# Kernel optimization log

Measured on AMD Instinct MI355X. Metric: run time of the kernel, lower is better.

Reference implementation:

```python
import jax, jax.numpy as jnp
from jax import lax
import numpy as np

OBJECT_W, BCE_W, DICE_W = 2.0, 5.0, 5.0
B, N, M, C = 8, 128, 32, 65536


def setup_inputs() -> dict:
    key = jax.random.key(0)
    k1, k2, k3 = jax.random.split(key, 3)
    objectness = jax.random.normal(k1, (B, N), jnp.float32)
    pred_masks = jax.random.normal(k2, (B, N, C), jnp.float32)
    gt_masks = jax.random.randint(k3, (B, M, C), 0, 2).astype(jnp.float32)
    return {"objectness": objectness, "pred_masks": pred_masks, "gt_masks": gt_masks}


def _cost_matrices(objectness, pred, gt):
    # BCE-with-logits vs all-ones target: log(1+exp(-x)) = softplus(-x)
    # BCE-with-logits vs all-zeros target: softplus(x)
    sp_pos = jax.nn.softplus(-pred)                       # [B,N,C]
    sp_neg = jax.nn.softplus(pred)                        # [B,N,C]
    # einsum('nc,mc->nm', pos, t) + einsum('nc,mc->nm', neg, 1-t), batched.
    # neg @ (1-t) = neg.sum(c) - neg @ t (avoids materializing 1-t).
    bce = (jnp.einsum('bnc,bmc->bnm', sp_pos, gt)
           + sp_neg.sum(-1)[:, :, None]
           - jnp.einsum('bnc,bmc->bnm', sp_neg, gt)) / pred.shape[-1]
    s = jax.nn.sigmoid(pred)
    numerator = 2.0 * jnp.einsum('bnc,bmc->bnm', s, gt)
    denominator = s.sum(-1)[:, :, None] + gt.sum(-1)[:, None, :]
    dice = 1.0 - (numerator + 1.0) / (denominator + 1.0)
    obj = -jax.nn.sigmoid(objectness)[:, :, None]         # [B,N,1]
    return OBJECT_W * obj + BCE_W * bce + DICE_W * dice    # [B,N,M]


def _lsap(cost):
    """Jonker-Volgenant shortest-augmenting-path LSAP (scipy algorithm).
    cost: [R, C] with R <= C. Returns col4row [R] int32: column per row."""
    R, Cn = cost.shape
    BIG = jnp.float32(1e30)

    def outer(cur_row, carry):
        u, v, row4col, col4row = carry
        shortest = jnp.full((Cn,), BIG, jnp.float32)
        path = jnp.full((Cn,), -1, jnp.int32)
        SR = jnp.zeros((R,), bool)
        SC = jnp.zeros((Cn,), bool)

        def sp_cond(s):
            return s[6] < 0

        def sp_body(s):
            i, shortest, path, SR, SC, minVal, sink = s
            SR = SR.at[i].set(True)
            d = minVal + cost[i] - u[i] - v
            better = (d < shortest) & (~SC)
            shortest = jnp.where(better, d, shortest)
            path = jnp.where(better, i, path)
            masked = jnp.where(SC, BIG, shortest)
            j = jnp.argmin(masked).astype(jnp.int32)
            minVal = masked[j]
            SC = SC.at[j].set(True)
            nxt = row4col[j]
            sink = jnp.where(nxt == -1, j, jnp.int32(-1))
            i = jnp.where(nxt == -1, i, nxt)
            return (i, shortest, path, SR, SC, minVal, sink)

        init = (cur_row.astype(jnp.int32), shortest, path, SR, SC,
                jnp.float32(0.0), jnp.int32(-1))
        i, shortest, path, SR, SC, minVal, sink = lax.while_loop(sp_cond, sp_body, init)

        # dual updates (scipy rectangular_lsap)
        u = u.at[cur_row].add(minVal)
        extra = SR & (jnp.arange(R) != cur_row)
        sp_at_col = shortest[jnp.clip(col4row, 0, Cn - 1)]
        u = jnp.where(extra, u + minVal - sp_at_col, u)
        v = jnp.where(SC, v - (minVal - shortest), v)

        # augment along path
        def aug_cond(s):
            return ~s[3]

        def aug_body(s):
            j, row4col, col4row, done = s
            i = path[j]
            row4col = row4col.at[j].set(i)
            tmp = col4row[i]
            col4row = col4row.at[i].set(j)
            done = (i == cur_row)
            return (tmp, row4col, col4row, done)

        _, row4col, col4row, _ = lax.while_loop(
            aug_cond, aug_body, (sink, row4col, col4row, jnp.array(False)))
        return (u, v, row4col, col4row)

    carry = (jnp.zeros((R,), jnp.float32), jnp.zeros((Cn,), jnp.float32),
             jnp.full((Cn,), -1, jnp.int32), jnp.full((R,), -1, jnp.int32))
    u, v, row4col, col4row = lax.fori_loop(0, R, outer, carry)
    return col4row


def reference(objectness, pred_masks, gt_masks):
    cost = _cost_matrices(objectness, pred_masks, gt_masks)   # [B,N,M]
    # scipy lsap on [N,M] then sort by target == solving on cost.T [M,N]:
    # indices[b, m] = matched query index for target m.
    indices = jax.vmap(_lsap)(jnp.transpose(cost, (0, 2, 1)))  # [B,M]
    return cost, indices
```

## Files before the change

kernel.cpp:

```cpp
#include <hip/hip_runtime.h>
#include <hip/hip_bf16.h>

#define LOG2E 1.4426950408889634f
#define LN2   0.6931471805599453f

typedef __attribute__((ext_vector_type(8))) short short8;
typedef __attribute__((ext_vector_type(4))) float f32x4;

#define B_ 8
#define N_ 128
#define M_ 32
#define C_ 65536
#define KCHUNKS 32
#define KC (C_ / KCHUNKS)
#define BK 128
#define AST 136

__device__ __forceinline__ unsigned short f2bf(float f) {
  unsigned u = __builtin_bit_cast(unsigned, f);
  u += 0x7fffu + ((u >> 16) & 1u);
  return (unsigned short)(u >> 16);
}
__device__ __forceinline__ unsigned pack_rne(float lo, float hi) {
  return (unsigned)f2bf(lo) | ((unsigned)f2bf(hi) << 16);
}
__device__ __forceinline__ unsigned pack_trunc(float lo, float hi) {
  unsigned ul = __builtin_bit_cast(unsigned, lo);
  unsigned uh = __builtin_bit_cast(unsigned, hi);
  return (uh & 0xFFFF0000u) | (ul >> 16);
}

__global__ __launch_bounds__(512, 2) void cost_partial_kernel(
    const float* __restrict__ pred, const float* __restrict__ gt,
    float* __restrict__ xg, float* __restrict__ sg,
    float* __restrict__ spsum, float* __restrict__ ssum,
    float* __restrict__ gtsum)
{
  __shared__ unsigned short Asx[128 * AST];
  __shared__ unsigned short Ass[128 * AST];
  __shared__ unsigned short Bt[32 * AST];
  const int kc = blockIdx.x, b = blockIdx.y;
  const int tid = threadIdx.x;
  const int lane = tid & 63;
  const int wave = tid >> 6;
  const int quad = lane >> 4, lcol = lane & 15;
  const int prow = tid >> 2, pq = tid & 3;
  const int grow = tid >> 4, gh = tid & 15;
  const int c0 = kc * KC;

  const float* predB = pred + (size_t)b * N_ * C_ + (size_t)prow * C_ + c0;
  const float* gtB   = gt   + (size_t)b * M_ * C_ + (size_t)grow * C_ + c0;

  float spacc = 0.f, sacc = 0.f, gtacc = 0.f;
  f32x4 acc[2][2];
#pragma unroll
  for (int rt = 0; rt < 2; ++rt)
#pragma unroll
    for (int ct = 0; ct < 2; ++ct)
      acc[rt][ct] = (f32x4){0.f, 0.f, 0.f, 0.f};

  for (int ks = 0; ks < KC / BK; ++ks) {
    const int cb = ks * BK;
    float4 p[8];
#pragma unroll
    for (int i = 0; i < 8; ++i)
      p[i] = *(const float4*)(predB + cb + (i * 4 + pq) * 4);
    float4 g0 = *(const float4*)(gtB + cb + gh * 4);
    float4 g1 = *(const float4*)(gtB + cb + (gh + 16) * 4);

#pragma unroll
    for (int i = 0; i < 8; ++i) {
      float xs[4] = {p[i].x, p[i].y, p[i].z, p[i].w};
      float ss[4];
#pragma unroll
      for (int e = 0; e < 4; ++e) {
        float x = xs[e];
        float t = fminf(fmaxf(x * LOG2E, -80.f), 80.f);
        float e2 = __builtin_amdgcn_exp2f(t);
        float z = 1.f + e2;
        float s = e2 * __builtin_amdgcn_rcpf(z);
        spacc += __builtin_amdgcn_logf(z) * LN2;
        sacc += s;
        ss[e] = s;
      }
      uint2 ux = {pack_rne(xs[0], xs[1]), pack_rne(xs[2], xs[3])};
      uint2 us = {pack_rne(ss[0], ss[1]), pack_rne(ss[2], ss[3])};
      *(uint2*)&Asx[prow * AST + (i * 4 + pq) * 4] = ux;
      *(uint2*)&Ass[prow * AST + (i * 4 + pq) * 4] = us;
    }
    gtacc += g0.x + g0.y + g0.z + g0.w + g1.x + g1.y + g1.z + g1.w;
    *(uint2*)&Bt[grow * AST + gh * 4]      = (uint2){pack_trunc(g0.x, g0.y), pack_trunc(g0.z, g0.w)};
    *(uint2*)&Bt[grow * AST + 64 + gh * 4] = (uint2){pack_trunc(g1.x, g1.y), pack_trunc(g1.z, g1.w)};
    __syncthreads();

    const unsigned short* Abase = (wave < 4) ? &Asx[(wave * 32) * AST]
                                             : &Ass[((wave - 4) * 32) * AST];
#pragma unroll
    for (int k0 = 0; k0 < BK; k0 += 32) {
      const int koff = k0 + quad * 8;
      short8 bf0 = *(const short8*)&Bt[lcol * AST + koff];
      short8 bf1 = *(const short8*)&Bt[(16 + lcol) * AST + koff];
#pragma unroll
      for (int rt = 0; rt < 2; ++rt) {
        short8 af = *(const short8*)&Abase[(rt * 16 + lcol) * AST + koff];
        acc[rt][0] = __builtin_amdgcn_mfma_f32_16x16x32_bf16(af, bf0, acc[rt][0], 0, 0, 0);
        acc[rt][1] = __builtin_amdgcn_mfma_f32_16x16x32_bf16(af, bf1, acc[rt][1], 0, 0, 0);
      }
    }
    __syncthreads();
  }

  spacc += __shfl_xor(spacc, 1); spacc += __shfl_xor(spacc, 2);
  sacc  += __shfl_xor(sacc, 1);  sacc  += __shfl_xor(sacc, 2);
  if (pq == 0) {
    atomicAdd(&spsum[b * N_ + prow], spacc);
    atomicAdd(&ssum[b * N_ + prow], sacc);
  }
  gtacc += __shfl_xor(gtacc, 1); gtacc += __shfl_xor(gtacc, 2);
  gtacc += __shfl_xor(gtacc, 4); gtacc += __shfl_xor(gtacc, 8);
  if (gh == 0) atomicAdd(&gtsum[b * M_ + grow], gtacc);

#pragma unroll
  for (int rt = 0; rt < 2; ++rt)
#pragma unroll
    for (int ct = 0; ct < 2; ++ct)
#pragma unroll
      for (int reg = 0; reg < 4; ++reg) {
        int r = (wave & 3) * 32 + rt * 16 + quad * 4 + reg;
        int ocol = ct * 16 + lcol;
        float v = acc[rt][ct][reg];
        float* dst = (wave < 4) ? xg : sg;
        atomicAdd(&dst[(b * N_ + r) * M_ + ocol], v);
      }
}

__global__ void finalize_kernel(const float* __restrict__ obj,
    const float* __restrict__ xg, const float* __restrict__ sg,
    const float* __restrict__ spsum, const float* __restrict__ ssum,
    const float* __restrict__ gtsum, float* __restrict__ cost)
{
  int idx = blockIdx.x * blockDim.x + threadIdx.x;
  int b = idx >> 12;
  int n = (idx >> 5) & 127;
  int m = idx & 31;
  float o = obj[b * N_ + n];
  float t = fminf(fmaxf(o * LOG2E, -80.f), 80.f);
  float e2 = __builtin_amdgcn_exp2f(t);
  float sig = e2 * __builtin_amdgcn_rcpf(1.f + e2);
  float bce = (spsum[b * N_ + n] - xg[idx]) * (1.0f / (float)C_);
  float dice = 1.f - (2.f * sg[idx] + 1.f) / (ssum[b * N_ + n] + gtsum[b * M_ + m] + 1.f);
  cost[idx] = -2.f * sig + 5.f * bce + 5.f * dice;
}

#define BIGF 1e30f

__device__ __forceinline__ float wave_min_all(float x) {
  const int BI = __builtin_bit_cast(int, BIGF);
  int v = __builtin_bit_cast(int, x);
#define MIN_STEP(ctrl)                                                        \
  {                                                                           \
    int t_ = __builtin_amdgcn_update_dpp(BI, v, ctrl, 0xf, 0xf, false);       \
    v = __builtin_bit_cast(int, fminf(__builtin_bit_cast(float, v),           \
                                      __builtin_bit_cast(float, t_)));        \
  }
  MIN_STEP(0x111)
  MIN_STEP(0x112)
  MIN_STEP(0x114)
  MIN_STEP(0x118)
  MIN_STEP(0x142)
  MIN_STEP(0x143)
#undef MIN_STEP
  return __builtin_bit_cast(float, __builtin_amdgcn_readlane(v, 63));
}

__device__ __forceinline__ float rdlane_f(float x, int l) {
  return __builtin_bit_cast(float, __builtin_amdgcn_readlane(__builtin_bit_cast(int, x), l));
}

__global__ __launch_bounds__(64) void lsap_kernel(const float* __restrict__ cost,
                                                  float* __restrict__ out)
{
  const int b = blockIdx.x;
  const int lane = threadIdx.x;
  __shared__ float cTs[M_ * 129];

#pragma unroll 4
  for (int t = 0; t < 16; ++t) {
    int e = t * 256 + lane * 4;
    float4 v4 = *(const float4*)&cost[b * 4096 + e];
    int n = e >> 5, m = e & 31;
    cTs[(m + 0) * 129 + n] = v4.x;
    cTs[(m + 1) * 129 + n] = v4.y;
    cTs[(m + 2) * 129 + n] = v4.z;
    cTs[(m + 3) * 129 + n] = v4.w;
  }
  __syncthreads();

  float u_reg = 0.f;
  int c4r = -1;
  float v0 = 0.f, v1 = 0.f;
  int r40 = -1, r41 = -1;

  for (int cur = 0; cur < M_; ++cur) {
    float sh0 = BIGF, sh1 = BIGF;
    int p0 = -1, p1 = -1;
    bool sc0 = false, sc1 = false;
    unsigned srmask = 0u;
    int i = cur, sink = -1;
    float minVal = 0.f;

    while (sink < 0) {
      srmask |= 1u << i;
      float ui = rdlane_f(u_reg, i);
      float cc0 = cTs[i * 129 + 2 * lane];
      float cc1 = cTs[i * 129 + 2 * lane + 1];
      float d0 = ((minVal + cc0) - ui) - v0;
      float d1 = ((minVal + cc1) - ui) - v1;
      if (!sc0 && d0 < sh0) { sh0 = d0; p0 = i; }
      if (!sc1 && d1 < sh1) { sh1 = d1; p1 = i; }
      float m0 = sc0 ? BIGF : sh0;
      float m1 = sc1 ? BIGF : sh1;
      float mv = wave_min_all(fminf(m0, m1));
      unsigned long long bl0 = __ballot(m0 == mv);
      unsigned long long bl1 = __ballot(m1 == mv);
      int j0 = bl0 ? 2 * (int)__builtin_ctzll(bl0) : 0x7fffffff;
      int j1 = bl1 ? 2 * (int)__builtin_ctzll(bl1) + 1 : 0x7fffffff;
      int j = j0 < j1 ? j0 : j1;
      minVal = mv;
      if (lane == (j >> 1)) { if (j & 1) sc1 = true; else sc0 = true; }
      int nxt = __builtin_amdgcn_readlane((j & 1) ? r41 : r40, j >> 1);
      if (nxt < 0) sink = j; else i = nxt;
    }

    int jj = c4r < 0 ? 0 : c4r;
    float g0 = __shfl(sh0, jj >> 1);
    float g1 = __shfl(sh1, jj >> 1);
    float sj = (jj & 1) ? g1 : g0;
    if (lane < M_) {
      if (lane == cur) u_reg += minVal;
      else if ((srmask >> lane) & 1u) u_reg += minVal - sj;
    }
    if (sc0) v0 -= minVal - sh0;
    if (sc1) v1 -= minVal - sh1;

    int j = sink;
    while (true) {
      int i2 = __builtin_amdgcn_readlane((j & 1) ? p1 : p0, j >> 1);
      if (lane == (j >> 1)) { if (j & 1) r41 = i2; else r40 = i2; }
      int tmp = __builtin_amdgcn_readlane(c4r, i2);
      if (lane == i2) c4r = j;
      if (i2 == cur) break;
      j = tmp;
    }
  }
  if (lane < M_) out[b * M_ + lane] = (float)c4r;
}

extern "C" void kernel_launch(void* const* d_in, const int* in_sizes, int n_in,
                              void* d_out, int out_size, void* d_ws, size_t ws_size,
                              hipStream_t stream)
{
  const float* obj  = (const float*)d_in[0];
  const float* pred = (const float*)d_in[1];
  const float* gt   = (const float*)d_in[2];
  float* out = (float*)d_out;

  float* xg    = (float*)d_ws;
  float* sg    = xg + 32768;
  float* spsum = sg + 32768;
  float* ssum  = spsum + 1024;
  float* gtsum = ssum + 1024;

  hipMemsetAsync(d_ws, 0, (size_t)(32768 * 2 + 1024 * 2 + 256) * sizeof(float), stream);
  cost_partial_kernel<<<dim3(KCHUNKS, B_), 512, 0, stream>>>(pred, gt, xg, sg, spsum, ssum, gtsum);
  finalize_kernel<<<dim3(32768 / 256), 256, 0, stream>>>(obj, xg, sg, spsum, ssum, gtsum, out);
  lsap_kernel<<<dim3(B_), 64, 0, stream>>>(out, out + 32768);
}
```

Measured before the change: 569.5 us.

## Replace atomic accumulation with per-chunk partial buffers and finer K split

Splits the C dimension into 64 chunks instead of 32 and uses 256-thread blocks, each wave computing 64 rows of a stacked [x;sigmoid] A tile. Each block now writes its partial Gram products and row and column sums to a private slab instead of issuing atomicAdds. The finalize kernel sums over the slabs, which also removes the memset. The aim is more blocks in flight and no atomic contention, at the cost of a larger workspace and a reduction pass reading 64 partial slabs.

```diff
diff --git a/kernel.cpp b/kernel.cpp
--- a/kernel.cpp
+++ b/kernel.cpp
@@ -11,10 +11,10 @@
 #define N_ 128
 #define M_ 32
 #define C_ 65536
-#define KCHUNKS 32
+#define KCHUNKS 64
 #define KC (C_ / KCHUNKS)
-#define BK 128
-#define AST 136
+#define BK 64
+#define AST 72
 
 __device__ __forceinline__ unsigned short f2bf(float f) {
   unsigned u = __builtin_bit_cast(unsigned, f);
@@ -30,31 +30,33 @@
   return (uh & 0xFFFF0000u) | (ul >> 16);
 }
 
-__global__ __launch_bounds__(512, 2) void cost_partial_kernel(
+__global__ __launch_bounds__(256, 2) void cost_partial_kernel(
     const float* __restrict__ pred, const float* __restrict__ gt,
-    float* __restrict__ xg, float* __restrict__ sg,
-    float* __restrict__ spsum, float* __restrict__ ssum,
-    float* __restrict__ gtsum)
+    float* __restrict__ xg_part, float* __restrict__ sg_part,
+    float* __restrict__ sp_part, float* __restrict__ ss_part,
+    float* __restrict__ gts_part)
 {
-  __shared__ unsigned short Asx[128 * AST];
-  __shared__ unsigned short Ass[128 * AST];
+  __shared__ unsigned short As[256 * AST];
   __shared__ unsigned short Bt[32 * AST];
   const int kc = blockIdx.x, b = blockIdx.y;
   const int tid = threadIdx.x;
-  const int lane = tid & 63;
-  const int wave = tid >> 6;
+  const int grp = tid >> 4, gl = tid & 15;
+  const int grow = tid >> 3, gh = tid & 7;
+  const int wave = tid >> 6, lane = tid & 63;
   const int quad = lane >> 4, lcol = lane & 15;
-  const int prow = tid >> 2, pq = tid & 3;
-  const int grow = tid >> 4, gh = tid & 15;
   const int c0 = kc * KC;
-
-  const float* predB = pred + (size_t)b * N_ * C_ + (size_t)prow * C_ + c0;
+  const int slab = kc * B_ + b;
+
+  const float* predB = pred + (size_t)b * N_ * C_ + c0;
   const float* gtB   = gt   + (size_t)b * M_ * C_ + (size_t)grow * C_ + c0;
 
-  float spacc = 0.f, sacc = 0.f, gtacc = 0.f;
-  f32x4 acc[2][2];
-#pragma unroll
-  for (int rt = 0; rt < 2; ++rt)
+  float spr[8], sr[8], gtacc = 0.f;
+#pragma unroll
+  for (int r = 0; r < 8; ++r) { spr[r] = 0.f; sr[r] = 0.f; }
+
+  f32x4 acc[4][2];
+#pragma unroll
+  for (int rt = 0; rt < 4; ++rt)
 #pragma unroll
     for (int ct = 0; ct < 2; ++ct)
       acc[rt][ct] = (f32x4){0.f, 0.f, 0.f, 0.f};
@@ -63,14 +65,15 @@
     const int cb = ks * BK;
     float4 p[8];
 #pragma unroll
-    for (int i = 0; i < 8; ++i)
-      p[i] = *(const float4*)(predB + cb + (i * 4 + pq) * 4);
+    for (int r = 0; r < 8; ++r)
+      p[r] = *(const float4*)(predB + (size_t)(r * 16 + grp) * C_ + cb + gl * 4);
     float4 g0 = *(const float4*)(gtB + cb + gh * 4);
-    float4 g1 = *(const float4*)(gtB + cb + (gh + 16) * 4);
-
-#pragma unroll
-    for (int i = 0; i < 8; ++i) {
-      float xs[4] = {p[i].x, p[i].y, p[i].z, p[i].w};
+    float4 g1 = *(const float4*)(gtB + cb + (gh + 8) * 4);
+
+#pragma unroll
+    for (int r = 0; r < 8; ++r) {
+      const int row = r * 16 + grp;
+      float xs[4] = {p[r].x, p[r].y, p[r].z, p[r].w};
       float ss[4];
 #pragma unroll
       for (int e = 0; e < 4; ++e) {
@@ -79,30 +82,30 @@
         float e2 = __builtin_amdgcn_exp2f(t);
         float z = 1.f + e2;
         float s = e2 * __builtin_amdgcn_rcpf(z);
-        spacc += __builtin_amdgcn_logf(z) * LN2;
-        sacc += s;
+        spr[r] += __builtin_amdgcn_logf(z) * LN2;
+        sr[r]  += s;
         ss[e] = s;
       }
-      uint2 ux = {pack_rne(xs[0], xs[1]), pack_rne(xs[2], xs[3])};
-      uint2 us = {pack_rne(ss[0], ss[1]), pack_rne(ss[2], ss[3])};
-      *(uint2*)&Asx[prow * AST + (i * 4 + pq) * 4] = ux;
-      *(uint2*)&Ass[prow * AST + (i * 4 + pq) * 4] = us;
+      *(uint2*)&As[row * AST + gl * 4] =
+          (uint2){pack_rne(xs[0], xs[1]), pack_rne(xs[2], xs[3])};
+      *(uint2*)&As[(N_ + row) * AST + gl * 4] =
+          (uint2){pack_rne(ss[0], ss[1]), pack_rne(ss[2], ss[3])};
     }
     gtacc += g0.x + g0.y + g0.z + g0.w + g1.x + g1.y + g1.z + g1.w;
-    *(uint2*)&Bt[grow * AST + gh * 4]      = (uint2){pack_trunc(g0.x, g0.y), pack_trunc(g0.z, g0.w)};
-    *(uint2*)&Bt[grow * AST + 64 + gh * 4] = (uint2){pack_trunc(g1.x, g1.y), pack_trunc(g1.z, g1.w)};
+    *(uint2*)&Bt[grow * AST + gh * 4] =
+        (uint2){pack_trunc(g0.x, g0.y), pack_trunc(g0.z, g0.w)};
+    *(uint2*)&Bt[grow * AST + (gh + 8) * 4] =
+        (uint2){pack_trunc(g1.x, g1.y), pack_trunc(g1.z, g1.w)};
     __syncthreads();
 
-    const unsigned short* Abase = (wave < 4) ? &Asx[(wave * 32) * AST]
-                                             : &Ass[((wave - 4) * 32) * AST];
 #pragma unroll
     for (int k0 = 0; k0 < BK; k0 += 32) {
       const int koff = k0 + quad * 8;
       short8 bf0 = *(const short8*)&Bt[lcol * AST + koff];
       short8 bf1 = *(const short8*)&Bt[(16 + lcol) * AST + koff];
 #pragma unroll
-      for (int rt = 0; rt < 2; ++rt) {
-        short8 af = *(const short8*)&Abase[(rt * 16 + lcol) * AST + koff];
+      for (int rt = 0; rt < 4; ++rt) {
+        short8 af = *(const short8*)&As[(wave * 64 + rt * 16 + lcol) * AST + koff];
         acc[rt][0] = __builtin_amdgcn_mfma_f32_16x16x32_bf16(af, bf0, acc[rt][0], 0, 0, 0);
         acc[rt][1] = __builtin_amdgcn_mfma_f32_16x16x32_bf16(af, bf1, acc[rt][1], 0, 0, 0);
       }
@@ -110,45 +113,63 @@
     __syncthreads();
   }
 
-  spacc += __shfl_xor(spacc, 1); spacc += __shfl_xor(spacc, 2);
-  sacc  += __shfl_xor(sacc, 1);  sacc  += __shfl_xor(sacc, 2);
-  if (pq == 0) {
-    atomicAdd(&spsum[b * N_ + prow], spacc);
-    atomicAdd(&ssum[b * N_ + prow], sacc);
-  }
-  gtacc += __shfl_xor(gtacc, 1); gtacc += __shfl_xor(gtacc, 2);
-  gtacc += __shfl_xor(gtacc, 4); gtacc += __shfl_xor(gtacc, 8);
-  if (gh == 0) atomicAdd(&gtsum[b * M_ + grow], gtacc);
-
-#pragma unroll
-  for (int rt = 0; rt < 2; ++rt)
+#pragma unroll
+  for (int r = 0; r < 8; ++r) {
+    float v1 = spr[r], v2 = sr[r];
+#pragma unroll
+    for (int off = 1; off < 16; off <<= 1) {
+      v1 += __shfl_xor(v1, off);
+      v2 += __shfl_xor(v2, off);
+    }
+    if (gl == 0) {
+      sp_part[slab * N_ + r * 16 + grp] = v1;
+      ss_part[slab * N_ + r * 16 + grp] = v2;
+    }
+  }
+  gtacc += __shfl_xor(gtacc, 1);
+  gtacc += __shfl_xor(gtacc, 2);
+  gtacc += __shfl_xor(gtacc, 4);
+  if (gh == 0) gts_part[slab * M_ + grow] = gtacc;
+
+#pragma unroll
+  for (int rt = 0; rt < 4; ++rt)
 #pragma unroll
     for (int ct = 0; ct < 2; ++ct)
 #pragma unroll
       for (int reg = 0; reg < 4; ++reg) {
-        int r = (wave & 3) * 32 + rt * 16 + quad * 4 + reg;
+        int orow = wave * 64 + rt * 16 + quad * 4 + reg;
         int ocol = ct * 16 + lcol;
         float v = acc[rt][ct][reg];
-        float* dst = (wave < 4) ? xg : sg;
-        atomicAdd(&dst[(b * N_ + r) * M_ + ocol], v);
+        if (orow < N_) xg_part[(slab * N_ + orow) * M_ + ocol] = v;
+        else           sg_part[(slab * N_ + (orow - N_)) * M_ + ocol] = v;
       }
 }
 
 __global__ void finalize_kernel(const float* __restrict__ obj,
-    const float* __restrict__ xg, const float* __restrict__ sg,
-    const float* __restrict__ spsum, const float* __restrict__ ssum,
-    const float* __restrict__ gtsum, float* __restrict__ cost)
+    const float* __restrict__ xg_part, const float* __restrict__ sg_part,
+    const float* __restrict__ sp_part, const float* __restrict__ ss_part,
+    const float* __restrict__ gts_part, float* __restrict__ cost)
 {
   int idx = blockIdx.x * blockDim.x + threadIdx.x;
   int b = idx >> 12;
   int n = (idx >> 5) & 127;
   int m = idx & 31;
+  float xa = 0.f, sa = 0.f, spa = 0.f, ssa = 0.f, ga = 0.f;
+#pragma unroll 4
+  for (int kc = 0; kc < KCHUNKS; ++kc) {
+    int slab = kc * B_ + b;
+    xa  += xg_part[(slab * N_ + n) * M_ + m];
+    sa  += sg_part[(slab * N_ + n) * M_ + m];
+    spa += sp_part[slab * N_ + n];
+    ssa += ss_part[slab * N_ + n];
+    ga  += gts_part[slab * M_ + m];
+  }
   float o = obj[b * N_ + n];
   float t = fminf(fmaxf(o * LOG2E, -80.f), 80.f);
   float e2 = __builtin_amdgcn_exp2f(t);
   float sig = e2 * __builtin_amdgcn_rcpf(1.f + e2);
-  float bce = (spsum[b * N_ + n] - xg[idx]) * (1.0f / (float)C_);
-  float dice = 1.f - (2.f * sg[idx] + 1.f) / (ssum[b * N_ + n] + gtsum[b * M_ + m] + 1.f);
+  float bce = (spa - xa) * (1.0f / (float)C_);
+  float dice = 1.f - (2.f * sa + 1.f) / (ssa + ga + 1.f);
   cost[idx] = -2.f * sig + 5.f * bce + 5.f * dice;
 }
 
@@ -265,14 +286,15 @@
   const float* gt   = (const float*)d_in[2];
   float* out = (float*)d_out;
 
-  float* xg    = (float*)d_ws;
-  float* sg    = xg + 32768;
-  float* spsum = sg + 32768;
-  float* ssum  = spsum + 1024;
-  float* gtsum = ssum + 1024;
-
-  hipMemsetAsync(d_ws, 0, (size_t)(32768 * 2 + 1024 * 2 + 256) * sizeof(float), stream);
-  cost_partial_kernel<<<dim3(KCHUNKS, B_), 512, 0, stream>>>(pred, gt, xg, sg, spsum, ssum, gtsum);
-  finalize_kernel<<<dim3(32768 / 256), 256, 0, stream>>>(obj, xg, sg, spsum, ssum, gtsum, out);
+  float* xg_part  = (float*)d_ws;
+  float* sg_part  = xg_part + (size_t)KCHUNKS * B_ * N_ * M_;
+  float* sp_part  = sg_part + (size_t)KCHUNKS * B_ * N_ * M_;
+  float* ss_part  = sp_part + (size_t)KCHUNKS * B_ * N_;
+  float* gts_part = ss_part + (size_t)KCHUNKS * B_ * N_;
+
+  cost_partial_kernel<<<dim3(KCHUNKS, B_), 256, 0, stream>>>(
+      pred, gt, xg_part, sg_part, sp_part, ss_part, gts_part);
+  finalize_kernel<<<dim3(32768 / 256), 256, 0, stream>>>(
+      obj, xg_part, sg_part, sp_part, ss_part, gts_part, out);
   lsap_kernel<<<dim3(B_), 64, 0, stream>>>(out, out + 32768);
 }
```

Result: no change. 569.3 us (-0.0%).
